# Optimization experiments

Measured on AMD Instinct MI355X. Metric: run time of the kernel, lower is better.

Reference implementation:

```python
import jax, jax.numpy as jnp
import numpy as np

B, S, D, H = 4, 2048, 1024, 16


def setup_inputs() -> dict:
    key = jax.random.key(0)
    ks = jax.random.split(key, 6)
    scale = 0.02
    return {
        "x": jax.random.normal(ks[0], (B, S, D), dtype=jnp.float32),
        "Wq": jax.random.normal(ks[1], (D, D), dtype=jnp.float32) * scale,
        "bq": jnp.zeros((D,), dtype=jnp.float32),
        "Wk": jax.random.normal(ks[2], (D, D), dtype=jnp.float32) * scale,
        "Wv": jax.random.normal(ks[3], (D, D), dtype=jnp.float32) * scale,
        "bv": jnp.zeros((D,), dtype=jnp.float32),
        "Wc": jax.random.normal(ks[4], (D, D), dtype=jnp.float32) * scale,
        "bc": jnp.zeros((D,), dtype=jnp.float32),
        "n_head": H,
    }


def reference(x, Wq, bq, Wk, Wv, bv, Wc, bc, n_head):
    # Projections (Conv1D == linear; k_proj has no bias since key_bias=False)
    q = x @ Wq + bq                      # [B, S, d_attn]
    k = x @ Wk                           # [B, S, d_attn]
    v = x @ Wv + bv                      # [B, S, d_attn]

    b, s, d_attn = q.shape
    d_head = d_attn // n_head
    # split heads -> [B, H, S, d_head]
    qh = q.reshape(b, s, n_head, d_head).transpose(0, 2, 1, 3)
    kh = k.reshape(b, s, n_head, d_head).transpose(0, 2, 1, 3)
    vh = v.reshape(b, s, n_head, d_head).transpose(0, 2, 1, 3)

    # scale applied to both q and k: 1/sqrt(sqrt(d_head))
    softmax_scale = 1.0 / np.sqrt(np.sqrt(d_head))
    qh = qh * softmax_scale
    kh = kh * softmax_scale

    w = jnp.einsum("bhqd,bhkd->bhqk", qh, kh)
    wtype = w.dtype
    w = w.astype(jnp.float32)
    n_q, n_k = w.shape[-2], w.shape[-1]
    # tril mask with diagonal offset n_k - n_q (supports incremental decode)
    mask = jnp.tril(jnp.ones((n_q, n_k), dtype=jnp.float32), k=n_k - n_q)[None, None]
    NEG = -1000000000.0
    w = w * mask + NEG * (1.0 - mask)
    w = jax.nn.softmax(w, axis=-1).astype(wtype)
    # attn_dropout rate 0 -> identity

    a = jnp.einsum("bhqk,bhkd->bhqd", w, vh)
    a = a.transpose(0, 2, 1, 3).reshape(b, s, d_attn)  # merge heads
    a = a @ Wc + bc
    # resid_dropout rate 0 -> identity
    hidden_state = jnp.stack([k, v])  # [2, B, S, d_attn]
    return (a, hidden_state)
```

## Files before the change

kernel.cpp:

```cpp
#include <hip/hip_runtime.h>
#include <stdint.h>

#define B_ 4
#define S_ 2048
#define D_ 1024
#define H_ 16
#define DH_ 64
#define MROWS (B_*S_)

typedef unsigned short ushortT;
typedef __attribute__((ext_vector_type(8))) short bf16x8;
typedef __attribute__((ext_vector_type(4))) float f32x4;

#define FLAG_BF16 1u
#define FLAG_F32  2u

__device__ __forceinline__ float b2f(ushortT u) {
  union { unsigned int i; float f; } v; v.i = ((unsigned int)u) << 16; return v.f;
}
__device__ __forceinline__ ushortT f2b(float f) {
  union { float f; unsigned int i; } v; v.f = f;
  unsigned int r = v.i + 0x7fffu + ((v.i >> 16) & 1u);
  return (ushortT)(r >> 16);
}

__device__ __forceinline__ float loadf(const ushortT* p) { return b2f(*p); }
__device__ __forceinline__ float loadf(const float* p)   { return *p; }
__device__ __forceinline__ unsigned int tob(ushortT u) { return u; }
__device__ __forceinline__ unsigned int tob(float f)   { return f2b(f); }

__device__ __forceinline__ void load8b(const ushortT* p, ushortT* u) {
  *(uint4*)u = *(const uint4*)p;
}
__device__ __forceinline__ void load8b(const float* p, ushortT* u) {
  float4 a = ((const float4*)p)[0], b = ((const float4*)p)[1];
  u[0] = f2b(a.x); u[1] = f2b(a.y); u[2] = f2b(a.z); u[3] = f2b(a.w);
  u[4] = f2b(b.x); u[5] = f2b(b.y); u[6] = f2b(b.z); u[7] = f2b(b.w);
}
template <typename T>
__device__ __forceinline__ void load16b(const T* p, ushortT* u) {
  load8b(p, u); load8b(p + 8, u + 8);
}

__device__ __forceinline__ void storef(ushortT* p, float v) { *p = f2b(v); }
__device__ __forceinline__ void storef(float* p, float v)   { *p = v; }

__device__ __forceinline__ void gload16(const ushortT* g, ushortT* l) {
  __builtin_amdgcn_global_load_lds(
      (const __attribute__((address_space(1))) void*)g,
      (__attribute__((address_space(3))) void*)l, 16, 0, 0);
}

__global__ void detect_dtype(const unsigned int* __restrict__ xw,
                             unsigned int* __restrict__ flag) {
  int lane = threadIdx.x;
  int cnt = 0;
  for (int i = lane; i < 2048; i += 64) {
    unsigned int e = (xw[i] >> 7) & 0xFFu;
    cnt += (e >= 0x68u && e <= 0x8Au) ? 1 : 0;
  }
#pragma unroll
  for (int off = 32; off; off >>= 1) cnt += __shfl_down(cnt, off);
  if (lane == 0) *flag = (cnt > 1024) ? FLAG_BF16 : FLAG_F32;
}

__global__ __launch_bounds__(256) void cvt_x_f32(
    const float* __restrict__ x, ushortT* __restrict__ xb,
    const unsigned int* __restrict__ flag) {
  if (*flag != FLAG_F32) return;
  const int total = MROWS * D_ / 8;
  for (int i = blockIdx.x * 256 + threadIdx.x; i < total; i += gridDim.x * 256) {
    float4 a = ((const float4*)x)[2 * i], b = ((const float4*)x)[2 * i + 1];
    ushortT u[8];
    u[0] = f2b(a.x); u[1] = f2b(a.y); u[2] = f2b(a.z); u[3] = f2b(a.w);
    u[4] = f2b(b.x); u[5] = f2b(b.y); u[6] = f2b(b.z); u[7] = f2b(b.w);
    ((uint4*)xb)[i] = *(uint4*)u;
  }
}

__global__ __launch_bounds__(256) void transpose_w(
    const void* W0, const void* W1, const void* W2, const void* W3,
    ushortT* dst0, ushortT* dstc, const unsigned int* flag) {
  __shared__ ushortT tile[64][72];
  int z = blockIdx.z;
  const void* W = (z == 0) ? W0 : (z == 1) ? W1 : (z == 2) ? W2 : W3;
  ushortT* dst = (z < 3) ? dst0 + (size_t)z * 1048576 : dstc;
  int n0 = blockIdx.x * 64, k0 = blockIdx.y * 64;
  int t = threadIdx.x;
  bool isb = (*flag == FLAG_BF16);
  for (int s = t; s < 512; s += 256) {
    int kr = s >> 3, nc = (s & 7) * 8;
    ushortT u[8];
    if (isb) load8b((const ushortT*)W + (size_t)(k0 + kr) * D_ + n0 + nc, u);
    else     load8b((const float*)W   + (size_t)(k0 + kr) * D_ + n0 + nc, u);
#pragma unroll
    for (int j = 0; j < 8; ++j) tile[kr][nc + j] = u[j];
  }
  __syncthreads();
  for (int s = t; s < 512; s += 256) {
    int nr = s >> 3, kc = (s & 7) * 8;
    ushortT u[8];
#pragma unroll
    for (int j = 0; j < 8; ++j) u[j] = tile[kc + j][nr];
    *(uint4*)(dst + (size_t)(n0 + nr) * D_ + k0 + kc) = *(uint4*)u;
  }
}

#define GEMM_BT_LDS (2 * 128 * 32)

template <typename TBIAS, typename TOUT>
__device__ __forceinline__ void gemm_bt(
    const ushortT* __restrict__ A, const ushortT* __restrict__ Bt,
    const TBIAS* __restrict__ bias, TOUT* __restrict__ C, ushortT* smem)
{
  const int K = 1024, N = 1024;
  ushortT* As = smem;
  ushortT* Bs = smem + 128 * 32;
  int m0 = blockIdx.x * 128;
  int n0 = blockIdx.y * 128;
  int t = threadIdx.x;
  int lane = t & 63;
  int w = t >> 6;
  int wm = w >> 1, wn = w & 1;

  f32x4 acc[4][4] = {};

  const ushortT* a_src0 = A  + (size_t)(m0 + (t >> 2)) * K + (t & 3) * 8;
  const ushortT* a_src1 = a_src0 + (size_t)64 * K;
  const ushortT* b_src0 = Bt + (size_t)(n0 + (t >> 2)) * K + (t & 3) * 8;
  const ushortT* b_src1 = b_src0 + (size_t)64 * K;
  ushortT* a_dst0 = &As[(16 * w) * 32];
  ushortT* a_dst1 = &As[(64 + 16 * w) * 32];
  ushortT* b_dst0 = &Bs[(16 * w) * 32];
  ushortT* b_dst1 = &Bs[(64 + 16 * w) * 32];

  for (int kt = 0; kt < K; kt += 32) {
    gload16(a_src0 + kt, a_dst0);
    gload16(a_src1 + kt, a_dst1);
    gload16(b_src0 + kt, b_dst0);
    gload16(b_src1 + kt, b_dst1);
    __syncthreads();

    int kq = (lane >> 4) * 8;
    int lm = lane & 15;
    bf16x8 af[4], bf[4];
#pragma unroll
    for (int mi = 0; mi < 4; ++mi)
      af[mi] = *(const bf16x8*)&As[(wm * 64 + mi * 16 + lm) * 32 + kq];
#pragma unroll
    for (int ni = 0; ni < 4; ++ni)
      bf[ni] = *(const bf16x8*)&Bs[(wn * 64 + ni * 16 + lm) * 32 + kq];
#pragma unroll
    for (int mi = 0; mi < 4; ++mi)
#pragma unroll
      for (int ni = 0; ni < 4; ++ni)
        acc[mi][ni] = __builtin_amdgcn_mfma_f32_16x16x32_bf16(af[mi], bf[ni], acc[mi][ni], 0, 0, 0);
    __syncthreads();
  }

#pragma unroll
  for (int ni = 0; ni < 4; ++ni) {
    int col = n0 + wn * 64 + ni * 16 + (lane & 15);
    float bvv = bias ? loadf(bias + col) : 0.f;
#pragma unroll
    for (int mi = 0; mi < 4; ++mi) {
      int rbase = m0 + wm * 64 + mi * 16 + ((lane >> 4) * 4);
#pragma unroll
      for (int r = 0; r < 4; ++r)
        storef(C + (size_t)(rbase + r) * N + col, acc[mi][ni][r] + bvv);
    }
  }
}

#define BK 32
#define BSTRIDE 40
#define GEMM_LDS (128 * BK + 128 * BSTRIDE)

template <typename TB, typename TOUT>
__device__ __forceinline__ void gemm_body(
    const ushortT* __restrict__ A, const TB* __restrict__ Bm,
    const TB* __restrict__ bias, TOUT* __restrict__ C, ushortT* smem)
{
  const int K = 1024, N = 1024;
  ushortT* As = smem;
  ushortT* Bs = smem + 128 * BK;
  int m0 = blockIdx.x * 128;
  int n0 = blockIdx.y * 128;
  int t = threadIdx.x;
  int lane = t & 63;
  int w = t >> 6;
  int wm = w >> 1, wn = w & 1;

  f32x4 acc[4][4] = {};

  const ushortT* a_src0 = A + (size_t)(m0 + (t >> 2)) * K + (t & 3) * 8;
  const ushortT* a_src1 = a_src0 + (size_t)64 * K;
  ushortT* a_dst0 = &As[(16 * w) * BK];
  ushortT* a_dst1 = &As[(64 + 16 * w) * BK];

  int cB = t & 127, r0 = (t >> 7) * 16;
  const TB* Bp0 = Bm + (size_t)r0 * N + n0 + cB;

  TB breg[16];
#pragma unroll
  for (int j = 0; j < 16; ++j) breg[j] = Bp0[(size_t)j * N];

  for (int kt = 0; kt < K; kt += BK) {
    gload16(a_src0 + kt, a_dst0);
    gload16(a_src1 + kt, a_dst1);
    {
      unsigned int* bd = (unsigned int*)&Bs[cB * BSTRIDE + r0];
#pragma unroll
      for (int j = 0; j < 8; ++j) {
        unsigned int lo = tob(breg[2 * j]);
        unsigned int hi = tob(breg[2 * j + 1]);
        bd[j] = lo | (hi << 16);
      }
    }
    __syncthreads();

    if (kt + BK < K) {
      const TB* bp = Bp0 + (size_t)(kt + BK) * N;
#pragma unroll
      for (int j = 0; j < 16; ++j) breg[j] = bp[(size_t)j * N];
    }

    int kq = (lane >> 4) * 8;
    int lm = lane & 15;
    bf16x8 af[4], bf[4];
#pragma unroll
    for (int mi = 0; mi < 4; ++mi)
      af[mi] = *(const bf16x8*)&As[(wm * 64 + mi * 16 + lm) * BK + kq];
#pragma unroll
    for (int ni = 0; ni < 4; ++ni)
      bf[ni] = *(const bf16x8*)&Bs[(wn * 64 + ni * 16 + lm) * BSTRIDE + kq];
#pragma unroll
    for (int mi = 0; mi < 4; ++mi)
#pragma unroll
      for (int ni = 0; ni < 4; ++ni)
        acc[mi][ni] = __builtin_amdgcn_mfma_f32_16x16x32_bf16(af[mi], bf[ni], acc[mi][ni], 0, 0, 0);
    __syncthreads();
  }

#pragma unroll
  for (int ni = 0; ni < 4; ++ni) {
    int col = n0 + wn * 64 + ni * 16 + (lane & 15);
    float bvv = bias ? loadf(bias + col) : 0.f;
#pragma unroll
    for (int mi = 0; mi < 4; ++mi) {
      int rbase = m0 + wm * 64 + mi * 16 + ((lane >> 4) * 4);
#pragma unroll
      for (int r = 0; r < 4; ++r)
        storef(C + (size_t)(rbase + r) * N + col, acc[mi][ni][r] + bvv);
    }
  }
}

#define KSTR 72
#define ATTN_LDS (2 * 64 * KSTR + 8 * 16 * KSTR)

template <typename TKV>
__device__ __forceinline__ void attn_body(
    const ushortT* __restrict__ Q, const TKV* __restrict__ Kh,
    const TKV* __restrict__ Vh, ushortT* __restrict__ O, ushortT* smem,
    int x, int h, int b)
{
  ushortT* Ks = smem;
  ushortT* Vs = smem + 64 * KSTR;
  ushortT* Ps = smem + 2 * 64 * KSTR;

  const int t = threadIdx.x, w = t >> 6, lane = t & 63;
  const int l15 = lane & 15, quad = lane >> 4;

  bf16x8 onesf;
  {
    ushortT u[8];
#pragma unroll
    for (int j = 0; j < 8; ++j) u[j] = 0x3F80;
    onesf = *(bf16x8*)u;
  }

  const TKV* kb = Kh + (size_t)(b * S_) * D_ + h * DH_;
  const TKV* vb = Vh + (size_t)(b * S_) * D_ + h * DH_;
  ushortT* Pw = Ps + w * (16 * KSTR);

  const int krow = t >> 3, kc = t & 7;
  const int vk = lane;

  for (int pi = 0; pi < 2; ++pi) {
    const int qt = pi ? (15 - x) : x;
    const int q0 = qt * 128;

    bf16x8 qf[2];
    {
      const ushortT* qp = Q + ((size_t)(b * S_) + q0 + w * 16 + l15) * D_ + h * DH_ + quad * 8;
#pragma unroll
      for (int c = 0; c < 2; ++c) {
        ushortT u[8];
        load8b(qp + c * 32, u);
        qf[c] = *(bf16x8*)u;
      }
    }

    f32x4 oac[4];
#pragma unroll
    for (int ni = 0; ni < 4; ++ni) oac[ni] = (f32x4){0.f, 0.f, 0.f, 0.f};
    f32x4 lac = (f32x4){0.f, 0.f, 0.f, 0.f};

    ushortT kr[8], vr[8];
    const int t0max = q0 + 64;

    {
      const TKV* kp = kb + (size_t)krow * D_ + kc * 8;
      load8b(kp, kr);
      const TKV* vp = vb + (size_t)vk * D_ + w * 8;
      load8b(vp, vr);
    }

    for (int t0 = 0; t0 <= t0max; t0 += 64) {
      *(uint4*)&Ks[krow * KSTR + kc * 8] = *(uint4*)kr;
#pragma unroll
      for (int j = 0; j < 8; ++j) Vs[(w * 8 + j) * KSTR + vk] = vr[j];
      __syncthreads();

      if (t0 + 64 <= t0max) {
        const TKV* kp = kb + (size_t)(t0 + 64 + krow) * D_ + kc * 8;
        load8b(kp, kr);
        const TKV* vp = vb + (size_t)(t0 + 64 + vk) * D_ + w * 8;
        load8b(vp, vr);
      }

      f32x4 sac[4];
#pragma unroll
      for (int ni = 0; ni < 4; ++ni) sac[ni] = (f32x4){0.f, 0.f, 0.f, 0.f};
      __builtin_amdgcn_s_setprio(1);
#pragma unroll
      for (int c = 0; c < 2; ++c)
#pragma unroll
        for (int ni = 0; ni < 4; ++ni) {
          bf16x8 bk = *(const bf16x8*)&Ks[(16 * ni + l15) * KSTR + c * 32 + quad * 8];
          sac[ni] = __builtin_amdgcn_mfma_f32_16x16x32_bf16(qf[c], bk, sac[ni], 0, 0, 0);
        }
      __builtin_amdgcn_s_setprio(0);

      if (t0 >= q0) {
        int koff = t0 - q0;
        int rowloc = w * 16 + quad * 4;
#pragma unroll
        for (int ni = 0; ni < 4; ++ni) {
          int kcol = koff + 16 * ni + l15;
#pragma unroll
          for (int r = 0; r < 4; ++r)
            if (kcol > rowloc + r) sac[ni][r] = -1e30f;
        }
      }

#pragma unroll
      for (int ni = 0; ni < 4; ++ni)
#pragma unroll
        for (int r = 0; r < 4; ++r) {
          float p = __expf(sac[ni][r] * 0.125f);
          Pw[(quad * 4 + r) * KSTR + 16 * ni + l15] = f2b(p);
        }

      __builtin_amdgcn_s_setprio(1);
#pragma unroll
      for (int c = 0; c < 2; ++c) {
        bf16x8 pa = *(const bf16x8*)&Pw[l15 * KSTR + c * 32 + quad * 8];
        lac = __builtin_amdgcn_mfma_f32_16x16x32_bf16(pa, onesf, lac, 0, 0, 0);
#pragma unroll
        for (int ni = 0; ni < 4; ++ni) {
          bf16x8 bv = *(const bf16x8*)&Vs[(16 * ni + l15) * KSTR + c * 32 + quad * 8];
          oac[ni] = __builtin_amdgcn_mfma_f32_16x16x32_bf16(pa, bv, oac[ni], 0, 0, 0);
        }
      }
      __builtin_amdgcn_s_setprio(0);
      __syncthreads();
    }

#pragma unroll
    for (int r = 0; r < 4; ++r) {
      float inv = 1.f / lac[r];
      ushortT* op = O + ((size_t)(b * S_) + q0 + w * 16 + quad * 4 + r) * D_ + h * DH_;
#pragma unroll
      for (int ni = 0; ni < 4; ++ni)
        op[16 * ni + l15] = f2b(oac[ni][r] * inv);
    }
  }
}

__global__ __launch_bounds__(256) void qkv_any(
    const void* x, const ushortT* wt, const void* bq, const void* bv,
    void* outp, const unsigned int* flag) {
  __shared__ __align__(16) ushortT smem[GEMM_BT_LDS];
  int z = blockIdx.z;
  const ushortT* Bt = wt + (size_t)z * 1048576;
  if (*flag == FLAG_BF16) {
    ushortT* o = (ushortT*)outp;
    const ushortT* A = (const ushortT*)x;
    if (z == 0)      gemm_bt<ushortT, ushortT>(A, Bt, (const ushortT*)bq, o, smem);
    else if (z == 1) gemm_bt<ushortT, ushortT>(A, Bt, nullptr, o + (size_t)8388608, smem);
    else             gemm_bt<ushortT, ushortT>(A, Bt, (const ushortT*)bv, o + (size_t)16777216, smem);
  } else {
    float* of = (float*)outp;
    const ushortT* A = (const ushortT*)outp;
    ushortT* q = (ushortT*)outp + (size_t)8388608;
    if (z == 0)      gemm_bt<float, ushortT>(A, Bt, (const float*)bq, q, smem);
    else if (z == 1) gemm_bt<float, float>(A, Bt, nullptr, of + (size_t)8388608, smem);
    else             gemm_bt<float, float>(A, Bt, (const float*)bv, of + (size_t)16777216, smem);
  }
}

__global__ __launch_bounds__(512, 2) void attn_any(
    void* outp, ushortT* O, const unsigned int* flag) {
  __shared__ __align__(16) ushortT smem[ATTN_LDS];
  int bid = (int)blockIdx.x + 8 * (int)blockIdx.y + 128 * (int)blockIdx.z;
  int lid = (bid & 7) * 64 + (bid >> 3);
  int x = lid & 7, h = (lid >> 3) & 15, b = lid >> 7;
  if (*flag == FLAG_BF16) {
    ushortT* o = (ushortT*)outp;
    attn_body<ushortT>(o, o + (size_t)8388608, o + (size_t)16777216, O, smem, x, h, b);
  } else {
    const ushortT* q = (const ushortT*)outp + (size_t)8388608;
    const float* of = (const float*)outp;
    attn_body<float>(q, of + (size_t)8388608, of + (size_t)16777216, O, smem, x, h, b);
  }
}

__global__ __launch_bounds__(256) void proj_bt(
    const ushortT* A, const ushortT* wct, const void* bc, void* outp,
    const unsigned int* flag) {
  __shared__ __align__(16) ushortT smem[GEMM_BT_LDS];
  if (*flag == FLAG_BF16)
    gemm_bt<ushortT, ushortT>(A, wct, (const ushortT*)bc, (ushortT*)outp, smem);
  else
    gemm_bt<float, float>(A, wct, (const float*)bc, (float*)outp, smem);
}

__global__ __launch_bounds__(256) void proj_legacy(
    const ushortT* A, const void* Wc, const void* bc, void* outp,
    const unsigned int* flag) {
  __shared__ __align__(16) ushortT smem[GEMM_LDS];
  if (*flag == FLAG_BF16)
    gemm_body<ushortT, ushortT>(A, (const ushortT*)Wc, (const ushortT*)bc, (ushortT*)outp, smem);
  else
    gemm_body<float, float>(A, (const float*)Wc, (const float*)bc, (float*)outp, smem);
}

extern "C" void kernel_launch(void* const* d_in, const int* in_sizes, int n_in,
                              void* d_out, int out_size, void* d_ws, size_t ws_size,
                              hipStream_t stream) {
  (void)in_sizes; (void)n_in; (void)out_size;

  unsigned int* flagp = (unsigned int*)d_ws;
  ushortT* attn_ws = (ushortT*)((char*)d_ws + 256);
  ushortT* wct_p = (ushortT*)((char*)d_ws + 256 + 16777216);
  bool wct_ok = ws_size >= (size_t)(256 + 16777216 + 2097152);

  detect_dtype<<<1, 64, 0, stream>>>((const unsigned int*)d_in[0], flagp);
  cvt_x_f32<<<2048, 256, 0, stream>>>((const float*)d_in[0], (ushortT*)d_out, flagp);

  dim3 gt(D_ / 64, D_ / 64, wct_ok ? 4 : 3);
  transpose_w<<<gt, 256, 0, stream>>>(d_in[1], d_in[3], d_in[4], d_in[6],
                                      attn_ws, wct_p, flagp);

  dim3 gq(MROWS / 128, D_ / 128, 3);
  dim3 gp(MROWS / 128, D_ / 128);
  dim3 ga(S_ / 256, H_, B_);

  qkv_any<<<gq, 256, 0, stream>>>(d_in[0], attn_ws, d_in[2], d_in[5], d_out, flagp);
  attn_any<<<ga, 512, 0, stream>>>(d_out, attn_ws, flagp);
  if (wct_ok)
    proj_bt<<<gp, 256, 0, stream>>>(attn_ws, wct_p, d_in[7], d_out, flagp);
  else
    proj_legacy<<<gp, 256, 0, stream>>>(attn_ws, d_in[6], d_in[7], d_out, flagp);
}
```

Before: 334.4 us.

## Pre-transpose V into bf16 head-major layout and stream it via LDS DMA

Adds a vt_build kernel that writes V per head as a transposed, XOR-swizzled bf16 layout. Attention then loads V tiles with global_load_lds into a double-buffered LDS region instead of scattering V element by element. Probabilities are packed with v_cvt_pk_bf16_f32 and written as wider stores. The cost is an extra launch and an extra pass over V, plus a fallback kernel launch that exits early when not needed. In the f32 path the transposed V overwrites the staging area at the start of the output.

```diff
diff --git a/kernel.cpp b/kernel.cpp
--- a/kernel.cpp
+++ b/kernel.cpp
@@ -23,6 +23,11 @@
   unsigned int r = v.i + 0x7fffu + ((v.i >> 16) & 1u);
   return (ushortT)(r >> 16);
 }
+__device__ __forceinline__ unsigned int cvtpk(float lo, float hi) {
+  unsigned int r;
+  asm("v_cvt_pk_bf16_f32 %0, %1, %2" : "=v"(r) : "v"(lo), "v"(hi));
+  return r;
+}
 
 __device__ __forceinline__ float loadf(const ushortT* p) { return b2f(*p); }
 __device__ __forceinline__ float loadf(const float* p)   { return *p; }
@@ -36,10 +41,6 @@
   float4 a = ((const float4*)p)[0], b = ((const float4*)p)[1];
   u[0] = f2b(a.x); u[1] = f2b(a.y); u[2] = f2b(a.z); u[3] = f2b(a.w);
   u[4] = f2b(b.x); u[5] = f2b(b.y); u[6] = f2b(b.z); u[7] = f2b(b.w);
-}
-template <typename T>
-__device__ __forceinline__ void load16b(const T* p, ushortT* u) {
-  load8b(p, u); load8b(p + 8, u + 8);
 }
 
 __device__ __forceinline__ void storef(ushortT* p, float v) { *p = f2b(v); }
@@ -106,6 +107,45 @@
   }
 }
 
+__global__ __launch_bounds__(256) void vt_build(
+    const void* outp, ushortT* vt_f32, ushortT* vt_b16,
+    const unsigned int* flag, int wvt_ok) {
+  __shared__ ushortT tile[64][72];
+  unsigned int fl = *flag;
+  if (fl == FLAG_BF16 && !wvt_ok) return;
+  ushortT* vt = (fl == FLAG_F32) ? vt_f32 : vt_b16;
+  int tile0 = blockIdx.x * 64, h = blockIdx.y, b = blockIdx.z;
+  int t = threadIdx.x;
+#pragma unroll
+  for (int pass = 0; pass < 2; ++pass) {
+    int s = (t >> 3) + pass * 32;
+    int d0 = (t & 7) * 8;
+    ushortT u[8];
+    if (fl == FLAG_F32)
+      load8b((const float*)outp + (size_t)16777216 +
+             ((size_t)(b * S_) + tile0 + s) * D_ + h * DH_ + d0, u);
+    else
+      load8b((const ushortT*)outp + (size_t)16777216 +
+             ((size_t)(b * S_) + tile0 + s) * D_ + h * DH_ + d0, u);
+#pragma unroll
+    for (int j = 0; j < 8; ++j) tile[s][d0 + j] = u[j];
+  }
+  __syncthreads();
+  int d = t >> 2;
+  int pg = (t & 3) * 16;
+  ushortT u[16];
+#pragma unroll
+  for (int j = 0; j < 16; ++j) {
+    int pp = pg + j;
+    int p = (((pp >> 3) ^ (d & 7)) << 3) | (pp & 7);
+    int s = ((p & 3) << 4) | (p >> 2);
+    u[j] = tile[s][d];
+  }
+  ushortT* dst = vt + ((size_t)((b * H_ + h) * DH_) + d) * S_ + tile0 + pg;
+  *(uint4*)dst = *(uint4*)&u[0];
+  *(uint4*)(dst + 8) = *(uint4*)&u[8];
+}
+
 #define GEMM_BT_LDS (2 * 128 * 32)
 
 template <typename TBIAS, typename TOUT>
@@ -256,11 +296,148 @@
   }
 }
 
+#define PSTR 72
+#define ATTN2_LDS (64 * 72 + 2 * 64 * 64 + 8 * 16 * PSTR)
+
+template <typename TK>
+__device__ __forceinline__ void attn_body2(
+    const ushortT* __restrict__ Q, const TK* __restrict__ Kh,
+    const ushortT* __restrict__ Vt, ushortT* __restrict__ O, ushortT* smem,
+    int x, int h, int b)
+{
+  ushortT* Ks = smem;
+  ushortT* Vs = smem + 64 * 72;
+  ushortT* Ps = smem + 64 * 72 + 2 * 64 * 64;
+
+  const int t = threadIdx.x, w = t >> 6, lane = t & 63;
+  const int l15 = lane & 15, quad = lane >> 4;
+
+  bf16x8 onesf;
+  {
+    ushortT u[8];
+#pragma unroll
+    for (int j = 0; j < 8; ++j) u[j] = 0x3F80;
+    onesf = *(bf16x8*)u;
+  }
+
+  const TK* kb = Kh + (size_t)(b * S_) * D_ + h * DH_;
+  const ushortT* vtb = Vt + (size_t)((b * H_ + h) * DH_) * S_;
+  ushortT* Pw = Ps + w * (16 * PSTR);
+
+  const int krow = t >> 3, kc = t & 7;
+  const ushortT* vsrc0 = vtb + (size_t)krow * S_ + kc * 8;
+
+  int cur = 0;
+  for (int pi = 0; pi < 2; ++pi) {
+    const int qt = pi ? (15 - x) : x;
+    const int q0 = qt * 128;
+
+    bf16x8 qf[2];
+    {
+      const ushortT* qp = Q + ((size_t)(b * S_) + q0 + w * 16 + l15) * D_ + h * DH_ + quad * 8;
+#pragma unroll
+      for (int c = 0; c < 2; ++c) {
+        ushortT u[8];
+        load8b(qp + c * 32, u);
+        qf[c] = *(bf16x8*)u;
+      }
+    }
+
+    f32x4 oac[4];
+#pragma unroll
+    for (int ni = 0; ni < 4; ++ni) oac[ni] = (f32x4){0.f, 0.f, 0.f, 0.f};
+    f32x4 lac = (f32x4){0.f, 0.f, 0.f, 0.f};
+
+    ushortT kr[8];
+    const int t0max = q0 + 64;
+
+    gload16(vsrc0, &Vs[cur * 4096 + w * 512]);
+    {
+      const TK* kp = kb + (size_t)krow * D_ + kc * 8;
+      load8b(kp, kr);
+    }
+
+    for (int t0 = 0; t0 <= t0max; t0 += 64) {
+      *(uint4*)&Ks[krow * 72 + kc * 8] = *(uint4*)kr;
+      __syncthreads();
+
+      if (t0 + 64 <= t0max) {
+        gload16(vsrc0 + (t0 + 64), &Vs[(cur ^ 1) * 4096 + w * 512]);
+        const TK* kp = kb + (size_t)(t0 + 64 + krow) * D_ + kc * 8;
+        load8b(kp, kr);
+      }
+
+      f32x4 sac[4];
+#pragma unroll
+      for (int ni = 0; ni < 4; ++ni) sac[ni] = (f32x4){0.f, 0.f, 0.f, 0.f};
+      __builtin_amdgcn_s_setprio(1);
+#pragma unroll
+      for (int c = 0; c < 2; ++c)
+#pragma unroll
+        for (int ni = 0; ni < 4; ++ni) {
+          bf16x8 bk = *(const bf16x8*)&Ks[(16 * ni + l15) * 72 + c * 32 + quad * 8];
+          sac[ni] = __builtin_amdgcn_mfma_f32_16x16x32_bf16(qf[c], bk, sac[ni], 0, 0, 0);
+        }
+      __builtin_amdgcn_s_setprio(0);
+
+      if (t0 >= q0) {
+        int koff = t0 - q0;
+        int rowloc = w * 16 + quad * 4;
+#pragma unroll
+        for (int ni = 0; ni < 4; ++ni) {
+          int kcol = koff + 16 * ni + l15;
+#pragma unroll
+          for (int r = 0; r < 4; ++r)
+            if (kcol > rowloc + r) sac[ni][r] = -1e30f;
+        }
+      }
+
+#pragma unroll
+      for (int r = 0; r < 4; ++r) {
+        float e0 = __expf(sac[0][r] * 0.125f);
+        float e1 = __expf(sac[1][r] * 0.125f);
+        float e2 = __expf(sac[2][r] * 0.125f);
+        float e3 = __expf(sac[3][r] * 0.125f);
+        uint2 pr;
+        pr.x = cvtpk(e0, e1);
+        pr.y = cvtpk(e2, e3);
+        *(uint2*)&Pw[(quad * 4 + r) * PSTR + 4 * l15] = pr;
+      }
+
+      const ushortT* Vsc = Vs + cur * 4096;
+      __builtin_amdgcn_s_setprio(1);
+#pragma unroll
+      for (int c = 0; c < 2; ++c) {
+        bf16x8 pa = *(const bf16x8*)&Pw[l15 * PSTR + c * 32 + quad * 8];
+        lac = __builtin_amdgcn_mfma_f32_16x16x32_bf16(pa, onesf, lac, 0, 0, 0);
+#pragma unroll
+        for (int ni = 0; ni < 4; ++ni) {
+          int d = 16 * ni + l15;
+          bf16x8 bv = *(const bf16x8*)&Vsc[d * 64 + ((((c << 2) + quad) ^ (d & 7)) << 3)];
+          oac[ni] = __builtin_amdgcn_mfma_f32_16x16x32_bf16(pa, bv, oac[ni], 0, 0, 0);
+        }
+      }
+      __builtin_amdgcn_s_setprio(0);
+      __syncthreads();
+      cur ^= 1;
+    }
+
+#pragma unroll
+    for (int r = 0; r < 4; ++r) {
+      float inv = 1.f / lac[r];
+      ushortT* op = O + ((size_t)(b * S_) + q0 + w * 16 + quad * 4 + r) * D_ + h * DH_;
+#pragma unroll
+      for (int ni = 0; ni < 4; ++ni)
+        op[16 * ni + l15] = f2b(oac[ni][r] * inv);
+    }
+  }
+}
+
 #define KSTR 72
-#define ATTN_LDS (2 * 64 * KSTR + 8 * 16 * KSTR)
+#define ATTN_FB_LDS (2 * 64 * KSTR + 8 * 16 * KSTR)
 
 template <typename TKV>
-__device__ __forceinline__ void attn_body(
+__device__ __forceinline__ void attn_body_fb(
     const ushortT* __restrict__ Q, const TKV* __restrict__ Kh,
     const TKV* __restrict__ Vh, ushortT* __restrict__ O, ushortT* smem,
     int x, int h, int b)
@@ -333,7 +510,6 @@
       f32x4 sac[4];
 #pragma unroll
       for (int ni = 0; ni < 4; ++ni) sac[ni] = (f32x4){0.f, 0.f, 0.f, 0.f};
-      __builtin_amdgcn_s_setprio(1);
 #pragma unroll
       for (int c = 0; c < 2; ++c)
 #pragma unroll
@@ -341,7 +517,6 @@
           bf16x8 bk = *(const bf16x8*)&Ks[(16 * ni + l15) * KSTR + c * 32 + quad * 8];
           sac[ni] = __builtin_amdgcn_mfma_f32_16x16x32_bf16(qf[c], bk, sac[ni], 0, 0, 0);
         }
-      __builtin_amdgcn_s_setprio(0);
 
       if (t0 >= q0) {
         int koff = t0 - q0;
@@ -363,7 +538,6 @@
           Pw[(quad * 4 + r) * KSTR + 16 * ni + l15] = f2b(p);
         }
 
-      __builtin_amdgcn_s_setprio(1);
 #pragma unroll
       for (int c = 0; c < 2; ++c) {
         bf16x8 pa = *(const bf16x8*)&Pw[l15 * KSTR + c * 32 + quad * 8];
@@ -374,7 +548,6 @@
           oac[ni] = __builtin_amdgcn_mfma_f32_16x16x32_bf16(pa, bv, oac[ni], 0, 0, 0);
         }
       }
-      __builtin_amdgcn_s_setprio(0);
       __syncthreads();
     }
 
@@ -412,19 +585,32 @@
 }
 
 __global__ __launch_bounds__(512, 2) void attn_any(
-    void* outp, ushortT* O, const unsigned int* flag) {
-  __shared__ __align__(16) ushortT smem[ATTN_LDS];
+    void* outp, ushortT* O, const unsigned int* flag,
+    const ushortT* vt_b16, int wvt_ok) {
+  __shared__ __align__(16) ushortT smem[ATTN2_LDS];
   int bid = (int)blockIdx.x + 8 * (int)blockIdx.y + 128 * (int)blockIdx.z;
   int lid = (bid & 7) * 64 + (bid >> 3);
   int x = lid & 7, h = (lid >> 3) & 15, b = lid >> 7;
   if (*flag == FLAG_BF16) {
-    ushortT* o = (ushortT*)outp;
-    attn_body<ushortT>(o, o + (size_t)8388608, o + (size_t)16777216, O, smem, x, h, b);
+    if (!wvt_ok) return;
+    const ushortT* o = (const ushortT*)outp;
+    attn_body2<ushortT>(o, o + (size_t)8388608, vt_b16, O, smem, x, h, b);
   } else {
     const ushortT* q = (const ushortT*)outp + (size_t)8388608;
     const float* of = (const float*)outp;
-    attn_body<float>(q, of + (size_t)8388608, of + (size_t)16777216, O, smem, x, h, b);
-  }
+    attn_body2<float>(q, of + (size_t)8388608, (const ushortT*)outp, O, smem, x, h, b);
+  }
+}
+
+__global__ __launch_bounds__(512, 2) void attn_fb(
+    void* outp, ushortT* O, const unsigned int* flag, int wvt_ok) {
+  __shared__ __align__(16) ushortT smem[ATTN_FB_LDS];
+  if (!(*flag == FLAG_BF16 && !wvt_ok)) return;
+  int bid = (int)blockIdx.x + 8 * (int)blockIdx.y + 128 * (int)blockIdx.z;
+  int lid = (bid & 7) * 64 + (bid >> 3);
+  int x = lid & 7, h = (lid >> 3) & 15, b = lid >> 7;
+  ushortT* o = (ushortT*)outp;
+  attn_body_fb<ushortT>(o, o + (size_t)8388608, o + (size_t)16777216, O, smem, x, h, b);
 }
 
 __global__ __launch_bounds__(256) void proj_bt(
@@ -455,7 +641,9 @@
   unsigned int* flagp = (unsigned int*)d_ws;
   ushortT* attn_ws = (ushortT*)((char*)d_ws + 256);
   ushortT* wct_p = (ushortT*)((char*)d_ws + 256 + 16777216);
+  ushortT* vtb16_p = (ushortT*)((char*)d_ws + 256 + 16777216 + 2097152);
   bool wct_ok = ws_size >= (size_t)(256 + 16777216 + 2097152);
+  int wvt_ok = ws_size >= (size_t)(256 + 16777216 + 2097152 + 16777216) ? 1 : 0;
 
   detect_dtype<<<1, 64, 0, stream>>>((const unsigned int*)d_in[0], flagp);
   cvt_x_f32<<<2048, 256, 0, stream>>>((const float*)d_in[0], (ushortT*)d_out, flagp);
@@ -465,11 +653,14 @@
                                       attn_ws, wct_p, flagp);
 
   dim3 gq(MROWS / 128, D_ / 128, 3);
+  dim3 gv(S_ / 64, H_, B_);
   dim3 gp(MROWS / 128, D_ / 128);
   dim3 ga(S_ / 256, H_, B_);
 
   qkv_any<<<gq, 256, 0, stream>>>(d_in[0], attn_ws, d_in[2], d_in[5], d_out, flagp);
-  attn_any<<<ga, 512, 0, stream>>>(d_out, attn_ws, flagp);
+  vt_build<<<gv, 256, 0, stream>>>(d_out, (ushortT*)d_out, vtb16_p, flagp, wvt_ok);
+  attn_any<<<ga, 512, 0, stream>>>(d_out, attn_ws, flagp, vtb16_p, wvt_ok);
+  attn_fb<<<ga, 512, 0, stream>>>(d_out, attn_ws, flagp, wvt_ok);
   if (wct_ok)
     proj_bt<<<gp, 256, 0, stream>>>(attn_ws, wct_p, d_in[7], d_out, flagp);
   else
```

Result: faster. 324.7 us (-2.9%).
